# Kernel tuning notes

Measured on AMD Instinct MI355X. Metric: run time of the kernel, lower is better.

Reference implementation:

```python
import jax, jax.numpy as jnp
import numpy as np

B, N, D = 2048, 101, 128
H = 8
ND = 1


def setup_inputs() -> dict:
    key = jax.random.key(0)
    ks = jax.random.split(key, 10)
    enc = jax.random.normal(ks[0], (B, N, D), jnp.float32)
    pool = jax.random.normal(ks[1], (B, D), jnp.float32)
    capcity = jnp.ones((B, 1), jnp.float32)
    # demands small relative to capacity so instances are feasible; depot demand = 0
    demand = jax.random.uniform(ks[2], (B, N), jnp.float32) * 0.05
    demand = demand.at[:, :ND].set(0.0)
    s = 1.0 / np.sqrt(D)
    return {
        'encoder_inputs': enc,
        'pool': pool,
        'capcity': capcity,
        'demand': demand,
        'n_steps': 150,
        'num_depots': ND,
        'T': 1,
        'fc_w': jax.random.normal(ks[3], (D, D + 1), jnp.float32) * s,
        'fc1_w': jax.random.normal(ks[4], (D, D), jnp.float32) * s,
        'pk_w': jax.random.normal(ks[5], (D, D), jnp.float32) * s,
        'mw_w': jax.random.normal(ks[6], (D, D), jnp.float32) * s,
        'mk_w': jax.random.normal(ks[7], (D, D), jnp.float32) * s,
        'mv_w': jax.random.normal(ks[8], (D, D), jnp.float32) * s,
        'mfc_w': jax.random.normal(ks[9], (D, D), jnp.float32) * s,
    }


def reference(encoder_inputs, pool, capcity, demand, n_steps, num_depots, T,
              fc_w, fc1_w, pk_w, mw_w, mk_w, mv_w, mfc_w):
    b, n, d = encoder_inputs.shape
    h = H
    hd = d // h
    norm_mha = 1.0 / np.sqrt(d / h)   # Attention1: 1/sqrt(head_dim)
    norm_prob = 1.0 / np.sqrt(d)      # ProbAttention: 1/sqrt(hidden_dim)
    nd = num_depots
    barange = jnp.arange(b)
    demands = demand.reshape(b, n)
    cap0 = jax.lax.stop_gradient(capcity[0, 0])  # capcity[0].item() in torch

    def update_mask(dyn_cap, index, mask1):
        # mark selected node visited
        mask1 = mask1.at[barange, index].set(1.0)
        go_depot = index < nd
        # depot masked only immediately after a depot visit (no idling at depot)
        mask1 = mask1.at[:, :nd].set(jnp.where(go_depot[:, None], 1.0, 0.0))
        # additionally mask customers whose demand exceeds remaining capacity
        mask = jnp.where(demands > dyn_cap, 1.0, mask1)
        # if every customer is masked, re-open the depot to keep softmax valid
        all_done = jnp.all(mask[:, nd:] > 0.5, axis=1)
        mask = mask.at[:, :nd].set(jnp.where(all_done[:, None], 0.0, mask[:, :nd]))
        return mask, mask1

    def update_state(dyn_cap, index):
        cur = demands[barange, index][:, None]
        new_cap = dyn_cap - cur
        new_cap = jnp.where((index < nd)[:, None], cap0, new_cap)
        return jax.lax.stop_gradient(new_cap)  # torch detaches capacity

    def prob_attention(state_t, mask):
        # ---- Attention1 (8-head masked attention, single query) ----
        Q = (state_t @ mw_w.T).reshape(b, h, hd)                              # bhd
        K = (encoder_inputs @ mk_w.T).reshape(b, n, h, hd).transpose(0, 2, 1, 3)  # bhnd
        V = (encoder_inputs @ mv_w.T).reshape(b, n, h, hd).transpose(0, 2, 1, 3)
        comp = norm_mha * jnp.einsum('bhd,bhnd->bhn', Q, K)
        comp = jnp.where(mask[:, None, :] > 0.5, -jnp.inf, comp)
        sc = jax.nn.softmax(comp, axis=-1)
        out = jnp.einsum('bhn,bhnd->bhd', sc, V).reshape(b, d) @ mfc_w.T
        # ---- tanh-clipped single-head pointer ----
        Kp = encoder_inputs @ pk_w.T
        comp2 = norm_prob * jnp.einsum('bd,bnd->bn', out, Kp)
        x = jnp.tanh(comp2) * 10.0
        logits = jnp.where(mask > 0.5, -jnp.inf, x) / T
        return logits

    dyn_cap0 = capcity.reshape(b, -1)
    mask1_init = jnp.zeros((b, n), encoder_inputs.dtype)
    mask0, mask1_0 = update_mask(dyn_cap0, jnp.zeros((b,), jnp.int32), mask1_init)
    input0 = encoder_inputs[:, 0, :]

    def step(carry, _):
        _input, pl, dyn_cap, mask, mask1 = carry
        dec = jnp.concatenate([_input, dyn_cap], axis=-1) @ fc_w.T
        pl = pl @ fc1_w.T  # torch reassigns pool = fc1(pool) every step
        dec = dec + pl
        logits = prob_attention(dec, mask)
        logp_all = jax.nn.log_softmax(logits, axis=-1)
        index = jnp.argmax(logits, axis=-1)  # greedy decoding (deterministic)
        log_p = logp_all[barange, index]
        is_done = (jnp.sum(mask1[:, 1:], axis=1) >= (n - 1)).astype(log_p.dtype)
        log_p = log_p * (1.0 - is_done)
        dyn_cap = update_state(dyn_cap, index)
        mask, mask1 = update_mask(dyn_cap, index, mask1)
        new_input = encoder_inputs[barange, index]
        return (new_input, pl, dyn_cap, mask, mask1), (index, log_p)

    carry0 = (input0, pool, dyn_cap0, mask0, mask1_0)
    _, (actions, log_ps) = jax.lax.scan(step, carry0, None, length=n_steps)
    actions = actions.T            # (b, n_steps)
    log_p = jnp.sum(log_ps, axis=0)  # (b,)
    return actions, log_p
```

## Files before the change

### kernel.cpp

```cpp
#include <hip/hip_runtime.h>

#define NNODE 101
#define DIM   128
#define NHEAD 8
#define NSTEP 150
#define BTOT  2048
#define ENCP  132

#define OFF_FCP   0
#define OFF_FC1P  16384
#define OFF_MWP   32768
#define OFF_MVP   49152
#define OFF_FP    65536
#define OFF_MKP   81920
#define OFF_FCC   98304
#define NORM_PROB 0.08838834764831845f

struct __align__(16) BS {
  float enc[NNODE * ENCP];
  float pl[DIM], dec[DIM], q[DIM], attn[DIM], op[DIM];
  float U[1888];
  float sc[1212];
  float mask[NNODE], mask1[NNODE], dem[NNODE];
  float cap, lp;
  int   idx;
};

#define EL(n,i)     S.enc[(n)*ENCP + (i)]
#define QK(h,i)     S.U[(h)*132 + (i)]
#define ZR(h,i)     S.U[(h)*132 + (i)]
#define CMP(h,n)    S.U[1056 + (h)*104 + (n)]
#define SC(n,h)     S.sc[(n)*12 + (h)]
#define SRED(n,k)   S.sc[(n)*12 + (k)]

__global__ void prep_weights(const float* __restrict__ fc_w,
                             const float* __restrict__ fc1_w,
                             const float* __restrict__ mw_w,
                             const float* __restrict__ mv_w,
                             const float* __restrict__ mfc_w,
                             const float* __restrict__ pk_w,
                             const float* __restrict__ mk_w,
                             float* __restrict__ ws) {
  int x = blockIdx.x * 256 + threadIdx.x;
  if (x < 4096) {
    int i4 = x >> 7, j = x & 127;
    float4 v = make_float4(fc_w[j * 129 + i4 * 4 + 0], fc_w[j * 129 + i4 * 4 + 1],
                           fc_w[j * 129 + i4 * 4 + 2], fc_w[j * 129 + i4 * 4 + 3]);
    *(float4*)&ws[OFF_FCP + x * 4] = v; return;
  }
  x -= 4096;
  if (x < 4096) {
    int i4 = x >> 7, j = x & 127;
    float4 v = make_float4(fc1_w[j * 128 + i4 * 4 + 0], fc1_w[j * 128 + i4 * 4 + 1],
                           fc1_w[j * 128 + i4 * 4 + 2], fc1_w[j * 128 + i4 * 4 + 3]);
    *(float4*)&ws[OFF_FC1P + x * 4] = v; return;
  }
  x -= 4096;
  if (x < 4096) {
    int i4 = x >> 7, j = x & 127;
    float4 v = make_float4(mw_w[j * 128 + i4 * 4 + 0], mw_w[j * 128 + i4 * 4 + 1],
                           mw_w[j * 128 + i4 * 4 + 2], mw_w[j * 128 + i4 * 4 + 3]);
    *(float4*)&ws[OFF_MWP + x * 4] = v; return;
  }
  x -= 4096;
  if (x < 4096) {
    int i4 = x >> 7, j = x & 127;
    float4 v = make_float4(mv_w[j * 128 + i4 * 4 + 0], mv_w[j * 128 + i4 * 4 + 1],
                           mv_w[j * 128 + i4 * 4 + 2], mv_w[j * 128 + i4 * 4 + 3]);
    *(float4*)&ws[OFF_MVP + x * 4] = v; return;
  }
  x -= 4096;
  if (x < 4096) {
    int i4 = x >> 7, j = x & 127;
    float a[4] = {0.f, 0.f, 0.f, 0.f};
    for (int d = 0; d < 128; ++d) {
      float p = pk_w[d * 128 + j];
      a[0] = fmaf(mfc_w[d * 128 + i4 * 4 + 0], p, a[0]);
      a[1] = fmaf(mfc_w[d * 128 + i4 * 4 + 1], p, a[1]);
      a[2] = fmaf(mfc_w[d * 128 + i4 * 4 + 2], p, a[2]);
      a[3] = fmaf(mfc_w[d * 128 + i4 * 4 + 3], p, a[3]);
    }
    *(float4*)&ws[OFF_FP + x * 4] = make_float4(a[0], a[1], a[2], a[3]); return;
  }
  x -= 4096;
  if (x < 4096) {
    int hk = x >> 7, j = x & 127;
    int h = hk >> 2, k4 = hk & 3;
    float4 v = make_float4(mk_w[(h * 16 + k4 * 4 + 0) * 128 + j],
                           mk_w[(h * 16 + k4 * 4 + 1) * 128 + j],
                           mk_w[(h * 16 + k4 * 4 + 2) * 128 + j],
                           mk_w[(h * 16 + k4 * 4 + 3) * 128 + j]);
    *(float4*)&ws[OFF_MKP + x * 4] = v; return;
  }
  x -= 4096;
  if (x < 128) ws[OFF_FCC + x] = fc_w[x * 129 + 128];
}

__global__ __launch_bounds__(256, 2) void decoder_loop(
    const float* __restrict__ enc, const float* __restrict__ pool,
    const float* __restrict__ capcity, const float* __restrict__ demand,
    const float* __restrict__ ws, float* __restrict__ d_out) {
  const float4* fcP  = (const float4*)(ws + OFF_FCP);
  const float4* fc1P = (const float4*)(ws + OFF_FC1P);
  const float4* mwP  = (const float4*)(ws + OFF_MWP);
  const float4* mvP  = (const float4*)(ws + OFF_MVP);
  const float4* FP   = (const float4*)(ws + OFF_FP);
  const float4* mkP  = (const float4*)(ws + OFF_MKP);

  __shared__ BS S;

  const int tl   = threadIdx.x;
  const int j    = tl & 127;
  const int half = tl >> 7;
  const int myb  = blockIdx.x;
  const float NEG_INF = -__builtin_inff();
  const float cap0 = capcity[0];

  {
    const float* src = enc + (size_t)myb * NNODE * DIM;
    for (int x = tl; x < NNODE * 32; x += 256) {
      int n = x >> 5, c = x & 31;
      *(float4*)&EL(n, c * 4) = *(const float4*)(src + (size_t)n * DIM + c * 4);
    }
  }
  __syncthreads();

  if (tl < 128) S.pl[tl] = pool[(size_t)myb * DIM + tl];
  if (tl < NNODE) S.dem[tl] = demand[(size_t)myb * NNODE + tl];
  if (tl == 0) { S.cap = capcity[myb]; S.lp = 0.f; S.idx = 0; }
  __syncthreads();
  if (tl < NNODE) {
    float v1 = (tl == 0) ? 1.f : 0.f;
    S.mask1[tl] = v1;
    S.mask[tl] = (S.dem[tl] > S.cap) ? 1.f : v1;
  }
  __syncthreads();
  if (tl < 64) {
    bool ok = (tl == 0) || (S.mask[tl] > 0.5f);
    if (tl + 64 < NNODE) ok = ok && (S.mask[tl + 64] > 0.5f);
    bool alld = __all(ok);
    if (alld && tl == 0) S.mask[0] = 0.f;
  }
  __syncthreads();

  for (int step = 0; step < NSTEP; ++step) {
    const float capR = S.cap;
    const int   cidx = S.idx;

    {
      const float4* x4 = (half == 0) ? (const float4*)&S.enc[cidx * ENCP]
                                     : (const float4*)&S.pl[0];
      const float4* wP = (half == 0) ? fcP : fc1P;
      float A = 0.f;
      #pragma unroll 8
      for (int t = 0; t < 32; ++t) {
        float4 v = x4[t];
        float4 wv = wP[t * 128 + j];
        A = fmaf(v.x, wv.x, A); A = fmaf(v.y, wv.y, A);
        A = fmaf(v.z, wv.z, A); A = fmaf(v.w, wv.w, A);
      }
      if (half == 0) A = fmaf(capR, ws[OFF_FCC + j], A);
      __syncthreads();
      if (half == 0) S.dec[j] = A;
      else           S.pl[j] = A;
    }
    __syncthreads();

    if (half == 0) {
      const float4* d4 = (const float4*)&S.dec[0];
      const float4* p4 = (const float4*)&S.pl[0];
      float B = 0.f;
      #pragma unroll 8
      for (int t = 0; t < 32; ++t) {
        float4 a = d4[t], p = p4[t];
        float4 wv = mwP[t * 128 + j];
        B = fmaf(a.x + p.x, wv.x, B); B = fmaf(a.y + p.y, wv.y, B);
        B = fmaf(a.z + p.z, wv.z, B); B = fmaf(a.w + p.w, wv.w, B);
      }
      S.q[j] = B;
    }
    __syncthreads();

    {
      const float4* q4 = (const float4*)&S.q[0];
      #pragma unroll
      for (int hh = 0; hh < 4; ++hh) {
        int h = half * 4 + hh;
        const float4* mp = mkP + (h * 4) * 128 + j;
        float4 M0 = mp[0], M1 = mp[128], M2 = mp[256], M3 = mp[384];
        float4 qa = q4[h * 4], qb = q4[h * 4 + 1], qc = q4[h * 4 + 2], qd4 = q4[h * 4 + 3];
        float acc = 0.f;
        acc = fmaf(qa.x, M0.x, acc); acc = fmaf(qa.y, M0.y, acc);
        acc = fmaf(qa.z, M0.z, acc); acc = fmaf(qa.w, M0.w, acc);
        acc = fmaf(qb.x, M1.x, acc); acc = fmaf(qb.y, M1.y, acc);
        acc = fmaf(qb.z, M1.z, acc); acc = fmaf(qb.w, M1.w, acc);
        acc = fmaf(qc.x, M2.x, acc); acc = fmaf(qc.y, M2.y, acc);
        acc = fmaf(qc.z, M2.z, acc); acc = fmaf(qc.w, M2.w, acc);
        acc = fmaf(qd4.x, M3.x, acc); acc = fmaf(qd4.y, M3.y, acc);
        acc = fmaf(qd4.z, M3.z, acc); acc = fmaf(qd4.w, M3.w, acc);
        QK(h, j) = acc;
      }
    }
    __syncthreads();

    {
      int h2 = tl & 3, nb = tl >> 2;
      int ha = h2 * 2, hb2 = h2 * 2 + 1;
      int n1 = nb + 64;
      bool has1 = (n1 < NNODE);
      float aA0 = 0.f, aB0 = 0.f, aA1 = 0.f, aB1 = 0.f;
      #pragma unroll 4
      for (int i4 = 0; i4 < 32; ++i4) {
        float4 qA = *(const float4*)&QK(ha,  i4 * 4);
        float4 qB = *(const float4*)&QK(hb2, i4 * 4);
        float4 e0 = *(const float4*)&EL(nb, i4 * 4);
        aA0 = fmaf(e0.x, qA.x, aA0); aA0 = fmaf(e0.y, qA.y, aA0);
        aA0 = fmaf(e0.z, qA.z, aA0); aA0 = fmaf(e0.w, qA.w, aA0);
        aB0 = fmaf(e0.x, qB.x, aB0); aB0 = fmaf(e0.y, qB.y, aB0);
        aB0 = fmaf(e0.z, qB.z, aB0); aB0 = fmaf(e0.w, qB.w, aB0);
        if (has1) {
          float4 e1 = *(const float4*)&EL(n1, i4 * 4);
          aA1 = fmaf(e1.x, qA.x, aA1); aA1 = fmaf(e1.y, qA.y, aA1);
          aA1 = fmaf(e1.z, qA.z, aA1); aA1 = fmaf(e1.w, qA.w, aA1);
          aB1 = fmaf(e1.x, qB.x, aB1); aB1 = fmaf(e1.y, qB.y, aB1);
          aB1 = fmaf(e1.z, qB.z, aB1); aB1 = fmaf(e1.w, qB.w, aB1);
        }
      }
      {
        float mk0 = S.mask[nb];
        CMP(ha,  nb) = (mk0 > 0.5f) ? NEG_INF : 0.25f * aA0;
        CMP(hb2, nb) = (mk0 > 0.5f) ? NEG_INF : 0.25f * aB0;
      }
      if (has1) {
        float mk1 = S.mask[n1];
        CMP(ha,  n1) = (mk1 > 0.5f) ? NEG_INF : 0.25f * aA1;
        CMP(hb2, n1) = (mk1 > 0.5f) ? NEG_INF : 0.25f * aB1;
      }
    }
    __syncthreads();

    {
      int w = tl >> 6, lane = tl & 63;
      int hb = w * 2;
      #pragma unroll
      for (int hh = 0; hh < 2; ++hh) {
        int h = hb + hh;
        float v0 = CMP(h, lane);
        float v1 = (lane < NNODE - 64) ? CMP(h, lane + 64) : NEG_INF;
        float m = fmaxf(v0, v1);
        #pragma unroll
        for (int o = 32; o > 0; o >>= 1) m = fmaxf(m, __shfl_xor(m, o, 64));
        float e0 = expf(v0 - m);
        float e1 = (lane < NNODE - 64) ? expf(v1 - m) : 0.f;
        float ss = e0 + e1;
        #pragma unroll
        for (int o = 32; o > 0; o >>= 1) ss += __shfl_xor(ss, o, 64);
        SC(lane, h) = e0 / ss;
        if (lane < NNODE - 64) SC(lane + 64, h) = e1 / ss;
      }
    }
    __syncthreads();

    {
      int j2 = tl & 63, hp = tl >> 6, hb = hp * 2;
      float a00 = 0.f, a01 = 0.f, a10 = 0.f, a11 = 0.f;
      #pragma unroll 4
      for (int n = 0; n < NNODE; ++n) {
        float2 s  = *(const float2*)&SC(n, hb);
        float2 ev = *(const float2*)&EL(n, j2 * 2);
        a00 = fmaf(s.x, ev.x, a00); a01 = fmaf(s.x, ev.y, a01);
        a10 = fmaf(s.y, ev.x, a10); a11 = fmaf(s.y, ev.y, a11);
      }
      *(float2*)&ZR(hb + 0, j2 * 2) = make_float2(a00, a01);
      *(float2*)&ZR(hb + 1, j2 * 2) = make_float2(a10, a11);
    }
    __syncthreads();

    if (half == 1) {
      int h = j >> 4;
      float C = 0.f;
      #pragma unroll 8
      for (int t = 0; t < 32; ++t) {
        float4 z = *(const float4*)&ZR(h, t * 4);
        float4 wv = mvP[t * 128 + j];
        C = fmaf(z.x, wv.x, C); C = fmaf(z.y, wv.y, C);
        C = fmaf(z.z, wv.z, C); C = fmaf(z.w, wv.w, C);
      }
      S.attn[j] = C;
    }
    __syncthreads();

    if (half == 0) {
      const float4* x4 = (const float4*)&S.attn[0];
      float D = 0.f;
      #pragma unroll 8
      for (int t = 0; t < 32; ++t) {
        float4 v = x4[t];
        float4 wv = FP[t * 128 + j];
        D = fmaf(v.x, wv.x, D); D = fmaf(v.y, wv.y, D);
        D = fmaf(v.z, wv.z, D); D = fmaf(v.w, wv.w, D);
      }
      S.op[j] = D;
    }
    __syncthreads();

    {
      int qd = tl & 3, nq = tl >> 2;
      #pragma unroll
      for (int p = 0; p < 2; ++p) {
        int n = p * 64 + nq;
        if (n < NNODE) {
          float acc = 0.f;
          #pragma unroll
          for (int i4 = 0; i4 < 8; ++i4) {
            float4 ov = *(const float4*)&S.op[qd * 32 + i4 * 4];
            float4 e4 = *(const float4*)&EL(n, qd * 32 + i4 * 4);
            acc = fmaf(e4.x, ov.x, acc);
            acc = fmaf(e4.y, ov.y, acc);
            acc = fmaf(e4.z, ov.z, acc);
            acc = fmaf(e4.w, ov.w, acc);
          }
          SRED(n, qd) = acc;
        }
      }
    }
    __syncthreads();

    if (tl < 64) {
      int lane = tl;
      float4 r0 = *(const float4*)&SRED(lane, 0);
      float tot0 = (r0.x + r0.y) + (r0.z + r0.w);
      float x0 = tanhf(tot0 * NORM_PROB) * 10.f;
      float v0 = (S.mask[lane] > 0.5f) ? NEG_INF : x0;
      float v1 = NEG_INF;
      if (lane < NNODE - 64) {
        float4 r1 = *(const float4*)&SRED(lane + 64, 0);
        float tot1 = (r1.x + r1.y) + (r1.z + r1.w);
        float x1 = tanhf(tot1 * NORM_PROB) * 10.f;
        v1 = (S.mask[lane + 64] > 0.5f) ? NEG_INF : x1;
      }
      float bv; int bi;
      if (v1 > v0) { bv = v1; bi = lane + 64; } else { bv = v0; bi = lane; }
      #pragma unroll
      for (int o = 32; o > 0; o >>= 1) {
        float ov = __shfl_xor(bv, o, 64);
        int   oi = __shfl_xor(bi, o, 64);
        if (ov > bv || (ov == bv && oi < bi)) { bv = ov; bi = oi; }
      }
      float e0 = expf(v0 - bv);
      float e1 = (lane < NNODE - 64) ? expf(v1 - bv) : 0.f;
      float ss = e0 + e1;
      #pragma unroll
      for (int o = 32; o > 0; o >>= 1) ss += __shfl_xor(ss, o, 64);
      int c = 0;
      if (lane >= 1 && S.mask1[lane] > 0.5f) c++;
      if (lane + 64 < NNODE && S.mask1[lane + 64] > 0.5f) c++;
      #pragma unroll
      for (int o = 32; o > 0; o >>= 1) c += __shfl_xor(c, o, 64);
      float newcap = (bi < 1) ? cap0 : (S.cap - S.dem[bi]);
      if (lane == 0) {
        if (c < NNODE - 1) S.lp += -logf(ss);
        d_out[(size_t)myb * NSTEP + step] = (float)bi;
        S.cap = newcap;
        S.idx = bi;
      }
      float m1a;
      if (lane == 0) m1a = (bi < 1) ? 1.f : 0.f;
      else           m1a = (lane == bi) ? 1.f : S.mask1[lane];
      float ma = (S.dem[lane] > newcap) ? 1.f : m1a;
      float m1b = 0.f, mb = 1.f;
      if (lane + 64 < NNODE) {
        m1b = (lane + 64 == bi) ? 1.f : S.mask1[lane + 64];
        mb  = (S.dem[lane + 64] > newcap) ? 1.f : m1b;
      }
      bool ok = (lane == 0) || (ma > 0.5f);
      if (lane + 64 < NNODE) ok = ok && (mb > 0.5f);
      bool alld = __all(ok);
      if (alld && lane == 0) ma = 0.f;
      S.mask1[lane] = m1a;
      S.mask[lane]  = ma;
      if (lane + 64 < NNODE) { S.mask1[lane + 64] = m1b; S.mask[lane + 64] = mb; }
    }
    __syncthreads();
  }

  if (tl == 0) d_out[(size_t)BTOT * NSTEP + myb] = S.lp;
}

extern "C" void kernel_launch(void* const* d_in, const int* in_sizes, int n_in,
                              void* d_out, int out_size, void* d_ws, size_t ws_size,
                              hipStream_t stream) {
  const float* enc   = (const float*)d_in[0];
  const float* pool  = (const float*)d_in[1];
  const float* cap   = (const float*)d_in[2];
  const float* dem   = (const float*)d_in[3];
  const float* fc_w  = (const float*)d_in[7];
  const float* fc1_w = (const float*)d_in[8];
  const float* pk_w  = (const float*)d_in[9];
  const float* mw_w  = (const float*)d_in[10];
  const float* mk_w  = (const float*)d_in[11];
  const float* mv_w  = (const float*)d_in[12];
  const float* mfc_w = (const float*)d_in[13];
  float* out = (float*)d_out;
  float* ws  = (float*)d_ws;

  prep_weights<<<97, 256, 0, stream>>>(fc_w, fc1_w, mw_w, mv_w, mfc_w, pk_w, mk_w, ws);
  decoder_loop<<<BTOT, 256, 0, stream>>>(enc, pool, cap, dem, ws, out);
}
```

Baseline: 9.424 ms.

## Double block size to 512 threads and split per-step work across more threads

Moves the decoder kernel from 256 to 512 threads per block and gives each thread less work in every phase. The score, softmax and attention phases go from two heads per thread to one, and the pool projection now runs in a separate thread quarter. A double-buffered pool vector removes one barrier from the first stage of each step. The aim is more parallelism per batch element to shorten the serial per-step latency. The cost is more idle threads in the matvec phases, where only 128 of 512 threads work, and higher register pressure under launch_bounds(512,4).

```diff
diff --git a/kernel.cpp b/kernel.cpp
--- a/kernel.cpp
+++ b/kernel.cpp
@@ -18,7 +18,8 @@
 
 struct __align__(16) BS {
   float enc[NNODE * ENCP];
-  float pl[DIM], dec[DIM], q[DIM], attn[DIM], op[DIM];
+  float pl[2][DIM];
+  float dec[DIM], q[DIM], attn[DIM], op[DIM];
   float U[1888];
   float sc[1212];
   float mask[NNODE], mask1[NNODE], dem[NNODE];
@@ -96,7 +97,7 @@
   if (x < 128) ws[OFF_FCC + x] = fc_w[x * 129 + 128];
 }
 
-__global__ __launch_bounds__(256, 2) void decoder_loop(
+__global__ __launch_bounds__(512, 4) void decoder_loop(
     const float* __restrict__ enc, const float* __restrict__ pool,
     const float* __restrict__ capcity, const float* __restrict__ demand,
     const float* __restrict__ ws, float* __restrict__ d_out) {
@@ -109,23 +110,23 @@
 
   __shared__ BS S;
 
-  const int tl   = threadIdx.x;
-  const int j    = tl & 127;
-  const int half = tl >> 7;
-  const int myb  = blockIdx.x;
+  const int tl  = threadIdx.x;
+  const int j   = tl & 127;
+  const int qr  = tl >> 7;
+  const int myb = blockIdx.x;
   const float NEG_INF = -__builtin_inff();
   const float cap0 = capcity[0];
 
   {
     const float* src = enc + (size_t)myb * NNODE * DIM;
-    for (int x = tl; x < NNODE * 32; x += 256) {
+    for (int x = tl; x < NNODE * 32; x += 512) {
       int n = x >> 5, c = x & 31;
       *(float4*)&EL(n, c * 4) = *(const float4*)(src + (size_t)n * DIM + c * 4);
     }
   }
   __syncthreads();
 
-  if (tl < 128) S.pl[tl] = pool[(size_t)myb * DIM + tl];
+  if (tl < 128) S.pl[0][tl] = pool[(size_t)myb * DIM + tl];
   if (tl < NNODE) S.dem[tl] = demand[(size_t)myb * NNODE + tl];
   if (tl == 0) { S.cap = capcity[myb]; S.lp = 0.f; S.idx = 0; }
   __syncthreads();
@@ -146,29 +147,37 @@
   for (int step = 0; step < NSTEP; ++step) {
     const float capR = S.cap;
     const int   cidx = S.idx;
-
-    {
-      const float4* x4 = (half == 0) ? (const float4*)&S.enc[cidx * ENCP]
-                                     : (const float4*)&S.pl[0];
-      const float4* wP = (half == 0) ? fcP : fc1P;
+    const int   pp   = step & 1;
+
+    if (qr == 0) {
+      const float4* x4 = (const float4*)&S.enc[cidx * ENCP];
       float A = 0.f;
       #pragma unroll 8
       for (int t = 0; t < 32; ++t) {
         float4 v = x4[t];
-        float4 wv = wP[t * 128 + j];
+        float4 wv = fcP[t * 128 + j];
         A = fmaf(v.x, wv.x, A); A = fmaf(v.y, wv.y, A);
         A = fmaf(v.z, wv.z, A); A = fmaf(v.w, wv.w, A);
       }
-      if (half == 0) A = fmaf(capR, ws[OFF_FCC + j], A);
-      __syncthreads();
-      if (half == 0) S.dec[j] = A;
-      else           S.pl[j] = A;
-    }
-    __syncthreads();
-
-    if (half == 0) {
+      A = fmaf(capR, ws[OFF_FCC + j], A);
+      S.dec[j] = A;
+    } else if (qr == 1) {
+      const float4* x4 = (const float4*)&S.pl[pp][0];
+      float A = 0.f;
+      #pragma unroll 8
+      for (int t = 0; t < 32; ++t) {
+        float4 v = x4[t];
+        float4 wv = fc1P[t * 128 + j];
+        A = fmaf(v.x, wv.x, A); A = fmaf(v.y, wv.y, A);
+        A = fmaf(v.z, wv.z, A); A = fmaf(v.w, wv.w, A);
+      }
+      S.pl[pp ^ 1][j] = A;
+    }
+    __syncthreads();
+
+    if (qr == 0) {
       const float4* d4 = (const float4*)&S.dec[0];
-      const float4* p4 = (const float4*)&S.pl[0];
+      const float4* p4 = (const float4*)&S.pl[pp ^ 1][0];
       float B = 0.f;
       #pragma unroll 8
       for (int t = 0; t < 32; ++t) {
@@ -184,8 +193,8 @@
     {
       const float4* q4 = (const float4*)&S.q[0];
       #pragma unroll
-      for (int hh = 0; hh < 4; ++hh) {
-        int h = half * 4 + hh;
+      for (int hh = 0; hh < 2; ++hh) {
+        int h = qr * 2 + hh;
         const float4* mp = mkP + (h * 4) * 128 + j;
         float4 M0 = mp[0], M1 = mp[128], M2 = mp[256], M3 = mp[384];
         float4 qa = q4[h * 4], qb = q4[h * 4 + 1], qc = q4[h * 4 + 2], qd4 = q4[h * 4 + 3];
@@ -204,79 +213,64 @@
     __syncthreads();
 
     {
-      int h2 = tl & 3, nb = tl >> 2;
-      int ha = h2 * 2, hb2 = h2 * 2 + 1;
+      int h = tl & 7, nb = tl >> 3;
       int n1 = nb + 64;
       bool has1 = (n1 < NNODE);
-      float aA0 = 0.f, aB0 = 0.f, aA1 = 0.f, aB1 = 0.f;
+      float a0 = 0.f, a1 = 0.f;
       #pragma unroll 4
       for (int i4 = 0; i4 < 32; ++i4) {
-        float4 qA = *(const float4*)&QK(ha,  i4 * 4);
-        float4 qB = *(const float4*)&QK(hb2, i4 * 4);
+        float4 qv = *(const float4*)&QK(h, i4 * 4);
         float4 e0 = *(const float4*)&EL(nb, i4 * 4);
-        aA0 = fmaf(e0.x, qA.x, aA0); aA0 = fmaf(e0.y, qA.y, aA0);
-        aA0 = fmaf(e0.z, qA.z, aA0); aA0 = fmaf(e0.w, qA.w, aA0);
-        aB0 = fmaf(e0.x, qB.x, aB0); aB0 = fmaf(e0.y, qB.y, aB0);
-        aB0 = fmaf(e0.z, qB.z, aB0); aB0 = fmaf(e0.w, qB.w, aB0);
+        a0 = fmaf(e0.x, qv.x, a0); a0 = fmaf(e0.y, qv.y, a0);
+        a0 = fmaf(e0.z, qv.z, a0); a0 = fmaf(e0.w, qv.w, a0);
         if (has1) {
           float4 e1 = *(const float4*)&EL(n1, i4 * 4);
-          aA1 = fmaf(e1.x, qA.x, aA1); aA1 = fmaf(e1.y, qA.y, aA1);
-          aA1 = fmaf(e1.z, qA.z, aA1); aA1 = fmaf(e1.w, qA.w, aA1);
-          aB1 = fmaf(e1.x, qB.x, aB1); aB1 = fmaf(e1.y, qB.y, aB1);
-          aB1 = fmaf(e1.z, qB.z, aB1); aB1 = fmaf(e1.w, qB.w, aB1);
+          a1 = fmaf(e1.x, qv.x, a1); a1 = fmaf(e1.y, qv.y, a1);
+          a1 = fmaf(e1.z, qv.z, a1); a1 = fmaf(e1.w, qv.w, a1);
         }
       }
       {
         float mk0 = S.mask[nb];
-        CMP(ha,  nb) = (mk0 > 0.5f) ? NEG_INF : 0.25f * aA0;
-        CMP(hb2, nb) = (mk0 > 0.5f) ? NEG_INF : 0.25f * aB0;
+        CMP(h, nb) = (mk0 > 0.5f) ? NEG_INF : 0.25f * a0;
       }
       if (has1) {
         float mk1 = S.mask[n1];
-        CMP(ha,  n1) = (mk1 > 0.5f) ? NEG_INF : 0.25f * aA1;
-        CMP(hb2, n1) = (mk1 > 0.5f) ? NEG_INF : 0.25f * aB1;
-      }
-    }
-    __syncthreads();
-
-    {
-      int w = tl >> 6, lane = tl & 63;
-      int hb = w * 2;
-      #pragma unroll
-      for (int hh = 0; hh < 2; ++hh) {
-        int h = hb + hh;
-        float v0 = CMP(h, lane);
-        float v1 = (lane < NNODE - 64) ? CMP(h, lane + 64) : NEG_INF;
-        float m = fmaxf(v0, v1);
-        #pragma unroll
-        for (int o = 32; o > 0; o >>= 1) m = fmaxf(m, __shfl_xor(m, o, 64));
-        float e0 = expf(v0 - m);
-        float e1 = (lane < NNODE - 64) ? expf(v1 - m) : 0.f;
-        float ss = e0 + e1;
-        #pragma unroll
-        for (int o = 32; o > 0; o >>= 1) ss += __shfl_xor(ss, o, 64);
-        SC(lane, h) = e0 / ss;
-        if (lane < NNODE - 64) SC(lane + 64, h) = e1 / ss;
-      }
-    }
-    __syncthreads();
-
-    {
-      int j2 = tl & 63, hp = tl >> 6, hb = hp * 2;
-      float a00 = 0.f, a01 = 0.f, a10 = 0.f, a11 = 0.f;
+        CMP(h, n1) = (mk1 > 0.5f) ? NEG_INF : 0.25f * a1;
+      }
+    }
+    __syncthreads();
+
+    {
+      int h = tl >> 6, lane = tl & 63;
+      float v0 = CMP(h, lane);
+      float v1 = (lane < NNODE - 64) ? CMP(h, lane + 64) : NEG_INF;
+      float m = fmaxf(v0, v1);
+      #pragma unroll
+      for (int o = 32; o > 0; o >>= 1) m = fmaxf(m, __shfl_xor(m, o, 64));
+      float e0 = expf(v0 - m);
+      float e1 = (lane < NNODE - 64) ? expf(v1 - m) : 0.f;
+      float ss = e0 + e1;
+      #pragma unroll
+      for (int o = 32; o > 0; o >>= 1) ss += __shfl_xor(ss, o, 64);
+      SC(lane, h) = e0 / ss;
+      if (lane < NNODE - 64) SC(lane + 64, h) = e1 / ss;
+    }
+    __syncthreads();
+
+    {
+      int j2 = tl & 63, h = tl >> 6;
+      float a00 = 0.f, a01 = 0.f;
       #pragma unroll 4
       for (int n = 0; n < NNODE; ++n) {
-        float2 s  = *(const float2*)&SC(n, hb);
+        float s   = SC(n, h);
         float2 ev = *(const float2*)&EL(n, j2 * 2);
-        a00 = fmaf(s.x, ev.x, a00); a01 = fmaf(s.x, ev.y, a01);
-        a10 = fmaf(s.y, ev.x, a10); a11 = fmaf(s.y, ev.y, a11);
-      }
-      *(float2*)&ZR(hb + 0, j2 * 2) = make_float2(a00, a01);
-      *(float2*)&ZR(hb + 1, j2 * 2) = make_float2(a10, a11);
-    }
-    __syncthreads();
-
-    if (half == 1) {
+        a00 = fmaf(s, ev.x, a00); a01 = fmaf(s, ev.y, a01);
+      }
+      *(float2*)&ZR(h, j2 * 2) = make_float2(a00, a01);
+    }
+    __syncthreads();
+
+    if (qr == 1) {
       int h = j >> 4;
       float C = 0.f;
       #pragma unroll 8
@@ -290,7 +284,7 @@
     }
     __syncthreads();
 
-    if (half == 0) {
+    if (qr == 0) {
       const float4* x4 = (const float4*)&S.attn[0];
       float D = 0.f;
       #pragma unroll 8
@@ -305,23 +299,19 @@
     __syncthreads();
 
     {
-      int qd = tl & 3, nq = tl >> 2;
-      #pragma unroll
-      for (int p = 0; p < 2; ++p) {
-        int n = p * 64 + nq;
-        if (n < NNODE) {
-          float acc = 0.f;
-          #pragma unroll
-          for (int i4 = 0; i4 < 8; ++i4) {
-            float4 ov = *(const float4*)&S.op[qd * 32 + i4 * 4];
-            float4 e4 = *(const float4*)&EL(n, qd * 32 + i4 * 4);
-            acc = fmaf(e4.x, ov.x, acc);
-            acc = fmaf(e4.y, ov.y, acc);
-            acc = fmaf(e4.z, ov.z, acc);
-            acc = fmaf(e4.w, ov.w, acc);
-          }
-          SRED(n, qd) = acc;
+      int qd = tl & 3, n = tl >> 2;
+      if (n < NNODE) {
+        float acc = 0.f;
+        #pragma unroll
+        for (int i4 = 0; i4 < 8; ++i4) {
+          float4 ov = *(const float4*)&S.op[qd * 32 + i4 * 4];
+          float4 e4 = *(const float4*)&EL(n, qd * 32 + i4 * 4);
+          acc = fmaf(e4.x, ov.x, acc);
+          acc = fmaf(e4.y, ov.y, acc);
+          acc = fmaf(e4.z, ov.z, acc);
+          acc = fmaf(e4.w, ov.w, acc);
         }
+        SRED(n, qd) = acc;
       }
     }
     __syncthreads();
@@ -405,5 +395,5 @@
   float* ws  = (float*)d_ws;
 
   prep_weights<<<97, 256, 0, stream>>>(fc_w, fc1_w, mw_w, mv_w, mfc_w, pk_w, mk_w, ws);
-  decoder_loop<<<BTOT, 256, 0, stream>>>(enc, pool, cap, dem, ws, out);
+  decoder_loop<<<BTOT, 512, 0, stream>>>(enc, pool, cap, dem, ws, out);
 }
```

After: 14.20 ms. 1.51x slower.

## Double-buffer pool vector and make score/softmax stages wave-local to drop barriers

Applied to the files above, without the earlier changes.

The pool vector is double-buffered by step parity, so the barrier before writing the fc1 output can be removed. The score computation is remapped so each wave owns two heads and all 101 nodes for them. This lets the block barriers after scoring and after softmax become wave-local LDS waitcnt fences. The aim is to cut block-wide synchronisations per decode step. The risk is correctness, because the softmax and the later weighted-sum stage may read data from other waves without a block barrier.

```diff
diff --git a/kernel.cpp b/kernel.cpp
--- a/kernel.cpp
+++ b/kernel.cpp
@@ -18,7 +18,8 @@
 
 struct __align__(16) BS {
   float enc[NNODE * ENCP];
-  float pl[DIM], dec[DIM], q[DIM], attn[DIM], op[DIM];
+  float pl[2][DIM];
+  float dec[DIM], q[DIM], attn[DIM], op[DIM];
   float U[1888];
   float sc[1212];
   float mask[NNODE], mask1[NNODE], dem[NNODE];
@@ -32,6 +33,8 @@
 #define CMP(h,n)    S.U[1056 + (h)*104 + (n)]
 #define SC(n,h)     S.sc[(n)*12 + (h)]
 #define SRED(n,k)   S.sc[(n)*12 + (k)]
+
+#define WAVE_FENCE() asm volatile("s_waitcnt lgkmcnt(0)" ::: "memory")
 
 __global__ void prep_weights(const float* __restrict__ fc_w,
                              const float* __restrict__ fc1_w,
@@ -125,7 +128,7 @@
   }
   __syncthreads();
 
-  if (tl < 128) S.pl[tl] = pool[(size_t)myb * DIM + tl];
+  if (tl < 128) S.pl[0][tl] = pool[(size_t)myb * DIM + tl];
   if (tl < NNODE) S.dem[tl] = demand[(size_t)myb * NNODE + tl];
   if (tl == 0) { S.cap = capcity[myb]; S.lp = 0.f; S.idx = 0; }
   __syncthreads();
@@ -146,10 +149,11 @@
   for (int step = 0; step < NSTEP; ++step) {
     const float capR = S.cap;
     const int   cidx = S.idx;
+    const int   pp   = step & 1;
 
     {
       const float4* x4 = (half == 0) ? (const float4*)&S.enc[cidx * ENCP]
-                                     : (const float4*)&S.pl[0];
+                                     : (const float4*)&S.pl[pp][0];
       const float4* wP = (half == 0) ? fcP : fc1P;
       float A = 0.f;
       #pragma unroll 8
@@ -160,15 +164,14 @@
         A = fmaf(v.z, wv.z, A); A = fmaf(v.w, wv.w, A);
       }
       if (half == 0) A = fmaf(capR, ws[OFF_FCC + j], A);
-      __syncthreads();
       if (half == 0) S.dec[j] = A;
-      else           S.pl[j] = A;
+      else           S.pl[pp ^ 1][j] = A;
     }
     __syncthreads();
 
     if (half == 0) {
       const float4* d4 = (const float4*)&S.dec[0];
-      const float4* p4 = (const float4*)&S.pl[0];
+      const float4* p4 = (const float4*)&S.pl[pp ^ 1][0];
       float B = 0.f;
       #pragma unroll 8
       for (int t = 0; t < 32; ++t) {
@@ -203,41 +206,39 @@
     }
     __syncthreads();
 
-    {
-      int h2 = tl & 3, nb = tl >> 2;
-      int ha = h2 * 2, hb2 = h2 * 2 + 1;
-      int n1 = nb + 64;
-      bool has1 = (n1 < NNODE);
-      float aA0 = 0.f, aB0 = 0.f, aA1 = 0.f, aB1 = 0.f;
+
+    {
+      int w = tl >> 6, l = tl & 63;
+      int h = 2 * w + (l >> 5), n0 = l & 31;
+      bool has3 = (n0 + 96 < NNODE);
+      float a0 = 0.f, a1 = 0.f, a2 = 0.f, a3 = 0.f;
       #pragma unroll 4
       for (int i4 = 0; i4 < 32; ++i4) {
-        float4 qA = *(const float4*)&QK(ha,  i4 * 4);
-        float4 qB = *(const float4*)&QK(hb2, i4 * 4);
-        float4 e0 = *(const float4*)&EL(nb, i4 * 4);
-        aA0 = fmaf(e0.x, qA.x, aA0); aA0 = fmaf(e0.y, qA.y, aA0);
-        aA0 = fmaf(e0.z, qA.z, aA0); aA0 = fmaf(e0.w, qA.w, aA0);
-        aB0 = fmaf(e0.x, qB.x, aB0); aB0 = fmaf(e0.y, qB.y, aB0);
-        aB0 = fmaf(e0.z, qB.z, aB0); aB0 = fmaf(e0.w, qB.w, aB0);
-        if (has1) {
-          float4 e1 = *(const float4*)&EL(n1, i4 * 4);
-          aA1 = fmaf(e1.x, qA.x, aA1); aA1 = fmaf(e1.y, qA.y, aA1);
-          aA1 = fmaf(e1.z, qA.z, aA1); aA1 = fmaf(e1.w, qA.w, aA1);
-          aB1 = fmaf(e1.x, qB.x, aB1); aB1 = fmaf(e1.y, qB.y, aB1);
-          aB1 = fmaf(e1.z, qB.z, aB1); aB1 = fmaf(e1.w, qB.w, aB1);
+        float4 qv = *(const float4*)&QK(h, i4 * 4);
+        float4 e0 = *(const float4*)&EL(n0,      i4 * 4);
+        float4 e1 = *(const float4*)&EL(n0 + 32, i4 * 4);
+        float4 e2 = *(const float4*)&EL(n0 + 64, i4 * 4);
+        a0 = fmaf(e0.x, qv.x, a0); a0 = fmaf(e0.y, qv.y, a0);
+        a0 = fmaf(e0.z, qv.z, a0); a0 = fmaf(e0.w, qv.w, a0);
+        a1 = fmaf(e1.x, qv.x, a1); a1 = fmaf(e1.y, qv.y, a1);
+        a1 = fmaf(e1.z, qv.z, a1); a1 = fmaf(e1.w, qv.w, a1);
+        a2 = fmaf(e2.x, qv.x, a2); a2 = fmaf(e2.y, qv.y, a2);
+        a2 = fmaf(e2.z, qv.z, a2); a2 = fmaf(e2.w, qv.w, a2);
+        if (has3) {
+          float4 e3 = *(const float4*)&EL(n0 + 96, i4 * 4);
+          a3 = fmaf(e3.x, qv.x, a3); a3 = fmaf(e3.y, qv.y, a3);
+          a3 = fmaf(e3.z, qv.z, a3); a3 = fmaf(e3.w, qv.w, a3);
         }
       }
-      {
-        float mk0 = S.mask[nb];
-        CMP(ha,  nb) = (mk0 > 0.5f) ? NEG_INF : 0.25f * aA0;
-        CMP(hb2, nb) = (mk0 > 0.5f) ? NEG_INF : 0.25f * aB0;
-      }
-      if (has1) {
-        float mk1 = S.mask[n1];
-        CMP(ha,  n1) = (mk1 > 0.5f) ? NEG_INF : 0.25f * aA1;
-        CMP(hb2, n1) = (mk1 > 0.5f) ? NEG_INF : 0.25f * aB1;
-      }
-    }
-    __syncthreads();
+      float mk;
+      mk = S.mask[n0];      CMP(h, n0)      = (mk > 0.5f) ? NEG_INF : 0.25f * a0;
+      mk = S.mask[n0 + 32]; CMP(h, n0 + 32) = (mk > 0.5f) ? NEG_INF : 0.25f * a1;
+      mk = S.mask[n0 + 64]; CMP(h, n0 + 64) = (mk > 0.5f) ? NEG_INF : 0.25f * a2;
+      if (has3) {
+        mk = S.mask[n0 + 96]; CMP(h, n0 + 96) = (mk > 0.5f) ? NEG_INF : 0.25f * a3;
+      }
+    }
+    WAVE_FENCE();
 
     {
       int w = tl >> 6, lane = tl & 63;
@@ -259,7 +260,7 @@
         if (lane < NNODE - 64) SC(lane + 64, h) = e1 / ss;
       }
     }
-    __syncthreads();
+    WAVE_FENCE();
 
     {
       int j2 = tl & 63, hp = tl >> 6, hb = hp * 2;
```

New measurement: 9.497 ms. Within noise of the previous version (+0.8%).
